# Performance work log

Measured on AMD Instinct MI355X. Metric: run time of the kernel, lower is better.

Reference implementation:

```python
import jax, jax.numpy as jnp
import numpy as np

BETA = 5.0  # init kwarg beta

def _row_normalize(x):
    # torch: diag(1/||x||_2) @ x  == row-wise L2 normalize (O(n*d), no n x n diag)
    return x / jnp.linalg.norm(x, axis=1, keepdims=True)

def _cluster(x, mu, num_iter, beta):
    # The torch code normalizes twice (before and after the init branch);
    # second normalize is idempotent but kept for faithfulness (cheap).
    x = _row_normalize(_row_normalize(x))
    for _ in range(num_iter):  # small fixed iteration count, not a data dim
        r = jax.nn.softmax(beta * (x @ mu.T), axis=1)      # [n, k]
        cluster_r = r.sum(axis=0)                          # [k]
        # torch: diag(1/cluster_r) @ (r.T @ x)  -> row scale of [k, d]
        mu = (r.T @ x) / cluster_r[:, None]                # [k, d]
    r = jax.nn.softmax(beta * (x @ mu.T), axis=1)
    return mu, r

def setup_inputs() -> dict:
    key = jax.random.key(0)
    k1, k2 = jax.random.split(key)
    x = jax.random.normal(k1, (100000, 512), dtype=jnp.float32)        # embeddings [n, d]
    init_mu = jax.random.uniform(k2, (128, 512), dtype=jnp.float32)    # self.init = rand(k, out_dim)
    return {"x": x, "init_mu": init_mu, "num_iter": 2}

def reference(x, init_mu, num_iter):
    mu_init, _ = _cluster(x, init_mu, num_iter, BETA)
    # torch: mu_init.detach().clone() -> stop_gradient
    mu, r = _cluster(x, jax.lax.stop_gradient(mu_init), 1, BETA)
    return (mu, r)
```

## Files before the change

kernel.cpp:

```cpp
#include <hip/hip_runtime.h>
#include <math.h>

constexpr int D = 512;
constexpr int KCL = 128;
constexpr float BETA_C = 5.0f;
constexpr int GSPLIT = 256;

typedef __attribute__((ext_vector_type(8))) short short8;
typedef __attribute__((ext_vector_type(4))) float f32x4;

typedef const __attribute__((address_space(1))) unsigned int* gptr_t;
typedef __attribute__((address_space(3))) unsigned int* sptr_t;

static __device__ __forceinline__ unsigned short f2bf(float f) {
    unsigned u = __builtin_bit_cast(unsigned, f);
    unsigned r = (u + 0x7FFFu + ((u >> 16) & 1u)) >> 16;
    return (unsigned short)r;
}
static __device__ __forceinline__ float bf2f(unsigned short h) {
    unsigned u = ((unsigned)h) << 16;
    return __builtin_bit_cast(float, u);
}
static __device__ __forceinline__ void split_bf(float v, unsigned short& h, unsigned short& lo) {
    h = f2bf(v);
    lo = f2bf(v - bf2f(h));
}

__global__ __launch_bounds__(256) void conv_x_kernel(const float* __restrict__ x,
        unsigned short* __restrict__ xh, unsigned short* __restrict__ xl,
        float* __restrict__ inv_norm, int n)
{
    int row  = blockIdx.x * 4 + (threadIdx.x >> 6);
    int lane = threadIdx.x & 63;
    if (row >= n) return;
    const float4* xr = reinterpret_cast<const float4*>(x + (size_t)row * D);
    float4 f0 = xr[lane];
    float4 f1 = xr[lane + 64];
    float s = f0.x*f0.x + f0.y*f0.y + f0.z*f0.z + f0.w*f0.w
            + f1.x*f1.x + f1.y*f1.y + f1.z*f1.z + f1.w*f1.w;
    #pragma unroll
    for (int m = 32; m; m >>= 1) s += __shfl_xor(s, m, 64);
    if (lane == 0) inv_norm[row] = 1.0f / sqrtf(s);

    ushort4 h0, l0, h1, l1;
    split_bf(f0.x, h0.x, l0.x); split_bf(f0.y, h0.y, l0.y);
    split_bf(f0.z, h0.z, l0.z); split_bf(f0.w, h0.w, l0.w);
    split_bf(f1.x, h1.x, l1.x); split_bf(f1.y, h1.y, l1.y);
    split_bf(f1.z, h1.z, l1.z); split_bf(f1.w, h1.w, l1.w);

    ushort4* xhr = reinterpret_cast<ushort4*>(xh + (size_t)row * D);
    ushort4* xlr = reinterpret_cast<ushort4*>(xl + (size_t)row * D);
    xhr[lane]      = h0;
    xhr[lane + 64] = h1;
    xlr[lane]      = l0;
    xlr[lane + 64] = l1;
}

__global__ __launch_bounds__(256) void conv_mu_kernel(const float* __restrict__ mu,
        unsigned short* __restrict__ mh, unsigned short* __restrict__ ml)
{
    int i = blockIdx.x * 256 + threadIdx.x;
    float4 v = reinterpret_cast<const float4*>(mu)[i];
    ushort4 h, l;
    split_bf(v.x, h.x, l.x); split_bf(v.y, h.y, l.y);
    split_bf(v.z, h.z, l.z); split_bf(v.w, h.w, l.w);
    reinterpret_cast<ushort4*>(mh)[i] = h;
    reinterpret_cast<ushort4*>(ml)[i] = l;
}

template<bool FIN>
__global__ __launch_bounds__(256) void passA_mfma_kernel(
    const unsigned short* __restrict__ xh, const unsigned short* __restrict__ xl,
    const unsigned short* __restrict__ mh, const unsigned short* __restrict__ ml,
    const float* __restrict__ inv_norm, float* __restrict__ r_out,
    float* __restrict__ cluster_r, int n)
{
    __shared__ unsigned short lds[4][128 * 32];
    __shared__ float part[4 * 128];

    const int t  = threadIdx.x;
    const int w  = t >> 6;
    const int l  = t & 63;
    const int fr = l & 15;
    const int fb = (l >> 4) * 8;
    const int rowBase = blockIdx.x * 128;

    f32x4 acc[2][8];
    #pragma unroll
    for (int m = 0; m < 2; ++m)
        #pragma unroll
        for (int nn = 0; nn < 8; ++nn) acc[m][nn] = (f32x4){0.f, 0.f, 0.f, 0.f};

    const unsigned short* pAh[2]; const unsigned short* pAl[2];
    const unsigned short* pBh[2]; const unsigned short* pBl[2];
    #pragma unroll
    for (int u = 0; u < 2; ++u) {
        int c = t + u * 256;
        int row = c >> 2;
        int kc  = (c & 3) * 8;
        int ga  = min(rowBase + row, n - 1);
        pAh[u] = xh + (size_t)ga * D + kc;
        pAl[u] = xl + (size_t)ga * D + kc;
        pBh[u] = mh + (size_t)row * D + kc;
        pBl[u] = ml + (size_t)row * D + kc;
    }

    for (int kb = 0; kb < D; kb += 32) {
        #pragma unroll
        for (int u = 0; u < 2; ++u) {
            int c = t + u * 256;
            __builtin_amdgcn_global_load_lds((gptr_t)pAh[u], (sptr_t)&lds[0][c * 8], 16, 0, 0);
            __builtin_amdgcn_global_load_lds((gptr_t)pAl[u], (sptr_t)&lds[1][c * 8], 16, 0, 0);
            __builtin_amdgcn_global_load_lds((gptr_t)pBh[u], (sptr_t)&lds[2][c * 8], 16, 0, 0);
            __builtin_amdgcn_global_load_lds((gptr_t)pBl[u], (sptr_t)&lds[3][c * 8], 16, 0, 0);
            pAh[u] += 32; pAl[u] += 32; pBh[u] += 32; pBl[u] += 32;
        }
        __syncthreads();

        short8 ah0 = *reinterpret_cast<const short8*>(&lds[0][(w * 32 +  0 + fr) * 32 + fb]);
        short8 ah1 = *reinterpret_cast<const short8*>(&lds[0][(w * 32 + 16 + fr) * 32 + fb]);
        short8 al0 = *reinterpret_cast<const short8*>(&lds[1][(w * 32 +  0 + fr) * 32 + fb]);
        short8 al1 = *reinterpret_cast<const short8*>(&lds[1][(w * 32 + 16 + fr) * 32 + fb]);
        #pragma unroll
        for (int nn = 0; nn < 8; ++nn) {
            short8 bh = *reinterpret_cast<const short8*>(&lds[2][(nn * 16 + fr) * 32 + fb]);
            short8 bl = *reinterpret_cast<const short8*>(&lds[3][(nn * 16 + fr) * 32 + fb]);
            acc[0][nn] = __builtin_amdgcn_mfma_f32_16x16x32_bf16(ah0, bh, acc[0][nn], 0, 0, 0);
            acc[1][nn] = __builtin_amdgcn_mfma_f32_16x16x32_bf16(ah1, bh, acc[1][nn], 0, 0, 0);
            acc[0][nn] = __builtin_amdgcn_mfma_f32_16x16x32_bf16(ah0, bl, acc[0][nn], 0, 0, 0);
            acc[1][nn] = __builtin_amdgcn_mfma_f32_16x16x32_bf16(ah1, bl, acc[1][nn], 0, 0, 0);
            acc[0][nn] = __builtin_amdgcn_mfma_f32_16x16x32_bf16(al0, bh, acc[0][nn], 0, 0, 0);
            acc[1][nn] = __builtin_amdgcn_mfma_f32_16x16x32_bf16(al1, bh, acc[1][nn], 0, 0, 0);
        }
        __syncthreads();
    }

    float csum[8];
    #pragma unroll
    for (int nn = 0; nn < 8; ++nn) csum[nn] = 0.f;

    #pragma unroll
    for (int m = 0; m < 2; ++m) {
        #pragma unroll
        for (int rr = 0; rr < 4; ++rr) {
            int row = rowBase + w * 32 + m * 16 + (l >> 4) * 4 + rr;
            bool valid = row < n;
            float sv = inv_norm[min(row, n - 1)];
            float bs = BETA_C * sv;
            float lg[8];
            float mx = -3.0e38f;
            #pragma unroll
            for (int nn = 0; nn < 8; ++nn) { lg[nn] = bs * acc[m][nn][rr]; mx = fmaxf(mx, lg[nn]); }
            #pragma unroll
            for (int sh = 1; sh < 16; sh <<= 1) mx = fmaxf(mx, __shfl_xor(mx, sh, 64));
            float e[8];
            float sum = 0.f;
            #pragma unroll
            for (int nn = 0; nn < 8; ++nn) { e[nn] = __expf(lg[nn] - mx); sum += e[nn]; }
            #pragma unroll
            for (int sh = 1; sh < 16; sh <<= 1) sum += __shfl_xor(sum, sh, 64);
            float rinv = 1.0f / sum;
            if (valid) {
                float* ro = r_out + (size_t)row * KCL + fr;
                if (!FIN) {
                    #pragma unroll
                    for (int nn = 0; nn < 8; ++nn) {
                        float rv = e[nn] * rinv;
                        csum[nn] += rv;
                        ro[nn * 16] = rv * sv;
                    }
                } else {
                    #pragma unroll
                    for (int nn = 0; nn < 8; ++nn) ro[nn * 16] = e[nn] * rinv;
                }
            }
        }
    }

    if (!FIN) {
        #pragma unroll
        for (int nn = 0; nn < 8; ++nn) {
            csum[nn] += __shfl_xor(csum[nn], 16, 64);
            csum[nn] += __shfl_xor(csum[nn], 32, 64);
        }
        if (l < 16) {
            #pragma unroll
            for (int nn = 0; nn < 8; ++nn) part[w * 128 + nn * 16 + l] = csum[nn];
        }
        __syncthreads();
        if (t < 128) {
            atomicAdd(&cluster_r[t], part[t] + part[128 + t] + part[256 + t] + part[384 + t]);
        }
    }
}

__global__ __launch_bounds__(256) void passB_kernel(
    const float* __restrict__ rp, const float* __restrict__ x,
    float* __restrict__ partials, int n, int chunk)
{
    __shared__ float Rs[32 * 132];
    __shared__ float Xs[32 * 132];

    const int t = threadIdx.x;
    const int a = t >> 4;
    const int b = t & 15;
    const int dbase = blockIdx.x * 128;
    const int r0 = blockIdx.y * chunk;
    const int r1 = min(n, r0 + chunk);

    float acc[8][8];
    #pragma unroll
    for (int i = 0; i < 8; ++i)
        #pragma unroll
        for (int j = 0; j < 8; ++j) acc[i][j] = 0.f;

    for (int ib = r0; ib < r1; ib += 32) {
        #pragma unroll
        for (int u = 0; u < 4; ++u) {
            int f  = t + u * 256;
            int ii = f >> 5;
            int c4 = (f & 31) << 2;
            int gr = ib + ii;
            float4 rv = make_float4(0.f, 0.f, 0.f, 0.f);
            float4 xv = make_float4(0.f, 0.f, 0.f, 0.f);
            if (gr < r1) {
                rv = *reinterpret_cast<const float4*>(rp + (size_t)gr * KCL + c4);
                xv = *reinterpret_cast<const float4*>(x + (size_t)gr * D + dbase + c4);
            }
            *reinterpret_cast<float4*>(&Rs[ii * 132 + c4]) = rv;
            *reinterpret_cast<float4*>(&Xs[ii * 132 + c4]) = xv;
        }
        __syncthreads();
        #pragma unroll 4
        for (int ii = 0; ii < 32; ++ii) {
            float4 rv0 = *reinterpret_cast<const float4*>(&Rs[ii * 132 + a * 8]);
            float4 rv1 = *reinterpret_cast<const float4*>(&Rs[ii * 132 + a * 8 + 4]);
            float4 xv0 = *reinterpret_cast<const float4*>(&Xs[ii * 132 + b * 4]);
            float4 xv1 = *reinterpret_cast<const float4*>(&Xs[ii * 132 + 64 + b * 4]);
            float rr[8] = {rv0.x, rv0.y, rv0.z, rv0.w, rv1.x, rv1.y, rv1.z, rv1.w};
            #pragma unroll
            for (int i = 0; i < 8; ++i) {
                acc[i][0] += rr[i] * xv0.x;
                acc[i][1] += rr[i] * xv0.y;
                acc[i][2] += rr[i] * xv0.z;
                acc[i][3] += rr[i] * xv0.w;
                acc[i][4] += rr[i] * xv1.x;
                acc[i][5] += rr[i] * xv1.y;
                acc[i][6] += rr[i] * xv1.z;
                acc[i][7] += rr[i] * xv1.w;
            }
        }
        __syncthreads();
    }

    float* pb = partials + (size_t)blockIdx.y * (KCL * D);
    #pragma unroll
    for (int i = 0; i < 8; ++i) {
        int c = a * 8 + i;
        float4 o0 = make_float4(acc[i][0], acc[i][1], acc[i][2], acc[i][3]);
        float4 o1 = make_float4(acc[i][4], acc[i][5], acc[i][6], acc[i][7]);
        *reinterpret_cast<float4*>(pb + (size_t)c * D + dbase + b * 4)      = o0;
        *reinterpret_cast<float4*>(pb + (size_t)c * D + dbase + 64 + b * 4) = o1;
    }
}

__global__ __launch_bounds__(256) void reduce_kernel(
    const float* __restrict__ partials, const float* __restrict__ cluster_r,
    float* __restrict__ mu_out, unsigned short* __restrict__ mh, unsigned short* __restrict__ ml)
{
    int idx = blockIdx.x * 256 + threadIdx.x;
    float s = 0.f;
    #pragma unroll 8
    for (int g = 0; g < GSPLIT; ++g) s += partials[(size_t)g * (KCL * D) + idx];
    int c = idx >> 9;
    float m = s / cluster_r[c];
    mu_out[idx] = m;
    unsigned short h, lo;
    split_bf(m, h, lo);
    mh[idx] = h;
    ml[idx] = lo;
}

extern "C" void kernel_launch(void* const* d_in, const int* in_sizes, int n_in,
                              void* d_out, int out_size, void* d_ws, size_t ws_size,
                              hipStream_t stream)
{
    const float* x   = (const float*)d_in[0];
    const float* mu0 = (const float*)d_in[1];
    const int n = in_sizes[0] / D;

    char* ws = (char*)d_ws;
    size_t off = 0;
    auto alloc = [&](size_t bytes) { size_t cur = off; off += (bytes + 255) & ~(size_t)255; return cur; };
    float*          inv_norm = (float*)(ws + alloc((size_t)n * 4));
    float*          r_ws     = (float*)(ws + alloc((size_t)n * KCL * 4));
    float*          parts    = (float*)(ws + alloc((size_t)GSPLIT * KCL * D * 4));
    float*          cr       = (float*)(ws + alloc(512));
    float*          mu_a     = (float*)(ws + alloc((size_t)KCL * D * 4));
    float*          mu_b     = (float*)(ws + alloc((size_t)KCL * D * 4));
    unsigned short* xh       = (unsigned short*)(ws + alloc((size_t)n * D * 2));
    unsigned short* xl       = (unsigned short*)(ws + alloc((size_t)n * D * 2));
    unsigned short* muh      = (unsigned short*)(ws + alloc((size_t)KCL * D * 2));
    unsigned short* mul      = (unsigned short*)(ws + alloc((size_t)KCL * D * 2));

    float* mu_final = (float*)d_out;
    float* r_final  = (float*)d_out + KCL * D;

    const int chunk   = (n + GSPLIT - 1) / GSPLIT;
    const int ablocks = (n + 127) / 128;

    conv_x_kernel<<<dim3((n + 3) / 4), 256, 0, stream>>>(x, xh, xl, inv_norm, n);
    conv_mu_kernel<<<dim3((KCL * D) / 1024), 256, 0, stream>>>(mu0, muh, mul);

    float* mu_tgt[3] = {mu_a, mu_b, mu_final};
    for (int it = 0; it < 3; ++it) {
        hipMemsetAsync(cr, 0, 512, stream);
        passA_mfma_kernel<false><<<dim3(ablocks), 256, 0, stream>>>(xh, xl, muh, mul, inv_norm, r_ws, cr, n);
        passB_kernel<<<dim3(4, GSPLIT), 256, 0, stream>>>(r_ws, x, parts, n, chunk);
        reduce_kernel<<<dim3((KCL * D) / 256), 256, 0, stream>>>(parts, cr, mu_tgt[it], muh, mul);
    }
    passA_mfma_kernel<true><<<dim3(ablocks), 256, 0, stream>>>(xh, xl, muh, mul, inv_norm, r_final, nullptr, n);
}
```

Measured before the change: 1.231 ms.

## Move r^T·x accumulation to split-bf16 MFMA with transposed packed operands

The FP32 FMA passB is replaced by an MFMA kernel that reads transposed, hi/lo-packed bf16 copies of r and x, computing r^T·x with three bf16 MFMAs per product. PassA now loads fp32 x directly and splits it on the fly, and its epilogue writes r transposed and packed through LDS. The precomputed xh/xl row-major buffers are dropped and the split count is halved. This is meant to remove the scalar FP32 GEMM cost of passB, at the price of an extra transpose-conversion pass, padding, and slightly reduced precision from the split-bf16 scheme.

```diff
diff --git a/kernel.cpp b/kernel.cpp
--- a/kernel.cpp
+++ b/kernel.cpp
@@ -4,7 +4,7 @@
 constexpr int D = 512;
 constexpr int KCL = 128;
 constexpr float BETA_C = 5.0f;
-constexpr int GSPLIT = 256;
+constexpr int SPLIT = 128;
 
 typedef __attribute__((ext_vector_type(8))) short short8;
 typedef __attribute__((ext_vector_type(4))) float f32x4;
@@ -21,39 +21,94 @@
     unsigned u = ((unsigned)h) << 16;
     return __builtin_bit_cast(float, u);
 }
-static __device__ __forceinline__ void split_bf(float v, unsigned short& h, unsigned short& lo) {
-    h = f2bf(v);
-    lo = f2bf(v - bf2f(h));
-}
-
-__global__ __launch_bounds__(256) void conv_x_kernel(const float* __restrict__ x,
-        unsigned short* __restrict__ xh, unsigned short* __restrict__ xl,
+static __device__ __forceinline__ unsigned pack_split(float v) {
+    unsigned short h = f2bf(v);
+    float hf = bf2f(h);
+    unsigned short lo = f2bf(v - hf);
+    return (unsigned)h | ((unsigned)lo << 16);
+}
+
+static __device__ __forceinline__ void split8(float4 a, float4 b, short8& hi, short8& lo) {
+    float v[8] = {a.x, a.y, a.z, a.w, b.x, b.y, b.z, b.w};
+    union { unsigned short us[8]; short8 s8; } H, L;
+    #pragma unroll
+    for (int j = 0; j < 8; ++j) {
+        unsigned short h = f2bf(v[j]);
+        float hf = bf2f(h);
+        H.us[j] = h;
+        L.us[j] = f2bf(v[j] - hf);
+    }
+    hi = H.s8; lo = L.s8;
+}
+
+static __device__ __forceinline__ void unpack8(uint4 a, uint4 b, short8& hi, short8& lo) {
+    union { unsigned u[4]; short8 s8; } H, L;
+    H.u[0] = (a.x & 0xFFFFu) | (a.y << 16);
+    H.u[1] = (a.z & 0xFFFFu) | (a.w << 16);
+    H.u[2] = (b.x & 0xFFFFu) | (b.y << 16);
+    H.u[3] = (b.z & 0xFFFFu) | (b.w << 16);
+    L.u[0] = (a.x >> 16) | (a.y & 0xFFFF0000u);
+    L.u[1] = (a.z >> 16) | (a.w & 0xFFFF0000u);
+    L.u[2] = (b.x >> 16) | (b.y & 0xFFFF0000u);
+    L.u[3] = (b.z >> 16) | (b.w & 0xFFFF0000u);
+    hi = H.s8; lo = L.s8;
+}
+
+__global__ __launch_bounds__(256) void conv_xT_kernel(const float* __restrict__ x,
+        unsigned* __restrict__ xt, float* __restrict__ normp, int n, int npad)
+{
+    __shared__ float tile[64 * 132];
+    const int t = threadIdx.x;
+    const int kbase = blockIdx.x * 64;
+    const int dbase = blockIdx.y * 128;
+
+    #pragma unroll
+    for (int u = 0; u < 8; ++u) {
+        int f = t + u * 256;
+        int row = f >> 5;
+        int c4 = (f & 31) << 2;
+        int gk = kbase + row;
+        float4 v = make_float4(0.f, 0.f, 0.f, 0.f);
+        if (gk < n) v = *reinterpret_cast<const float4*>(x + (size_t)gk * D + dbase + c4);
+        *reinterpret_cast<float4*>(&tile[row * 132 + c4]) = v;
+    }
+    __syncthreads();
+
+    if (t < 64) {
+        int gk = kbase + t;
+        if (gk < n) {
+            float s = 0.f;
+            #pragma unroll
+            for (int j = 0; j < 128; ++j) {
+                float v = tile[t * 132 + ((j + t) & 127)];
+                s += v * v;
+            }
+            normp[(size_t)blockIdx.y * n + gk] = s;
+        }
+    }
+
+    int dl = t >> 1, kh = t & 1;
+    size_t gb = (size_t)(dbase + dl) * npad + kbase + kh * 32;
+    #pragma unroll
+    for (int q = 0; q < 8; ++q) {
+        uint4 o;
+        unsigned* op = reinterpret_cast<unsigned*>(&o);
+        #pragma unroll
+        for (int j = 0; j < 4; ++j) {
+            float v = tile[(kh * 32 + q * 4 + j) * 132 + dl];
+            op[j] = pack_split(v);
+        }
+        *reinterpret_cast<uint4*>(xt + gb + q * 4) = o;
+    }
+}
+
+__global__ __launch_bounds__(256) void norm_fin_kernel(const float* __restrict__ normp,
         float* __restrict__ inv_norm, int n)
 {
-    int row  = blockIdx.x * 4 + (threadIdx.x >> 6);
-    int lane = threadIdx.x & 63;
-    if (row >= n) return;
-    const float4* xr = reinterpret_cast<const float4*>(x + (size_t)row * D);
-    float4 f0 = xr[lane];
-    float4 f1 = xr[lane + 64];
-    float s = f0.x*f0.x + f0.y*f0.y + f0.z*f0.z + f0.w*f0.w
-            + f1.x*f1.x + f1.y*f1.y + f1.z*f1.z + f1.w*f1.w;
-    #pragma unroll
-    for (int m = 32; m; m >>= 1) s += __shfl_xor(s, m, 64);
-    if (lane == 0) inv_norm[row] = 1.0f / sqrtf(s);
-
-    ushort4 h0, l0, h1, l1;
-    split_bf(f0.x, h0.x, l0.x); split_bf(f0.y, h0.y, l0.y);
-    split_bf(f0.z, h0.z, l0.z); split_bf(f0.w, h0.w, l0.w);
-    split_bf(f1.x, h1.x, l1.x); split_bf(f1.y, h1.y, l1.y);
-    split_bf(f1.z, h1.z, l1.z); split_bf(f1.w, h1.w, l1.w);
-
-    ushort4* xhr = reinterpret_cast<ushort4*>(xh + (size_t)row * D);
-    ushort4* xlr = reinterpret_cast<ushort4*>(xl + (size_t)row * D);
-    xhr[lane]      = h0;
-    xhr[lane + 64] = h1;
-    xlr[lane]      = l0;
-    xlr[lane + 64] = l1;
+    int i = blockIdx.x * 256 + threadIdx.x;
+    if (i < n)
+        inv_norm[i] = 1.0f / sqrtf(normp[i] + normp[(size_t)n + i] +
+                                   normp[2 * (size_t)n + i] + normp[3 * (size_t)n + i]);
 }
 
 __global__ __launch_bounds__(256) void conv_mu_kernel(const float* __restrict__ mu,
@@ -62,27 +117,44 @@
     int i = blockIdx.x * 256 + threadIdx.x;
     float4 v = reinterpret_cast<const float4*>(mu)[i];
     ushort4 h, l;
-    split_bf(v.x, h.x, l.x); split_bf(v.y, h.y, l.y);
-    split_bf(v.z, h.z, l.z); split_bf(v.w, h.w, l.w);
+    float hf;
+    h.x = f2bf(v.x); hf = bf2f(h.x); l.x = f2bf(v.x - hf);
+    h.y = f2bf(v.y); hf = bf2f(h.y); l.y = f2bf(v.y - hf);
+    h.z = f2bf(v.z); hf = bf2f(h.z); l.z = f2bf(v.z - hf);
+    h.w = f2bf(v.w); hf = bf2f(h.w); l.w = f2bf(v.w - hf);
     reinterpret_cast<ushort4*>(mh)[i] = h;
     reinterpret_cast<ushort4*>(ml)[i] = l;
 }
 
+__global__ __launch_bounds__(256) void pad_r_kernel(unsigned* __restrict__ rt, int npad, int k0)
+{
+    int cnt = npad - k0;
+    int idx = blockIdx.x * 256 + threadIdx.x;
+    if (idx < KCL * cnt) {
+        int cl = idx / cnt;
+        int k  = idx - cl * cnt;
+        rt[(size_t)cl * npad + k0 + k] = 0u;
+    }
+}
+
 template<bool FIN>
 __global__ __launch_bounds__(256) void passA_mfma_kernel(
-    const unsigned short* __restrict__ xh, const unsigned short* __restrict__ xl,
+    const float* __restrict__ x,
     const unsigned short* __restrict__ mh, const unsigned short* __restrict__ ml,
     const float* __restrict__ inv_norm, float* __restrict__ r_out,
-    float* __restrict__ cluster_r, int n)
-{
-    __shared__ unsigned short lds[4][128 * 32];
+    unsigned* __restrict__ r_tp, float* __restrict__ cluster_r, int n, int npad)
+{
+    __shared__ union {
+        struct { float a[128 * 32]; unsigned short bh[128 * 32]; unsigned short bl[128 * 32]; } c;
+        unsigned T[64 * 130];
+    } lds;
     __shared__ float part[4 * 128];
 
     const int t  = threadIdx.x;
     const int w  = t >> 6;
     const int l  = t & 63;
     const int fr = l & 15;
-    const int fb = (l >> 4) * 8;
+    const int g  = l >> 4;
     const int rowBase = blockIdx.x * 128;
 
     f32x4 acc[2][8];
@@ -91,40 +163,58 @@
         #pragma unroll
         for (int nn = 0; nn < 8; ++nn) acc[m][nn] = (f32x4){0.f, 0.f, 0.f, 0.f};
 
-    const unsigned short* pAh[2]; const unsigned short* pAl[2];
-    const unsigned short* pBh[2]; const unsigned short* pBl[2];
+    const float* pA[4];
+    const unsigned short* pBh[2];
+    const unsigned short* pBl[2];
+    #pragma unroll
+    for (int u = 0; u < 4; ++u) {
+        int c   = t + u * 256;
+        int row = c >> 3;
+        int ch  = c & 7;
+        int ga  = min(rowBase + row, n - 1);
+        pA[u] = x + (size_t)ga * D + ((ch ^ (row & 7)) << 2);
+    }
     #pragma unroll
     for (int u = 0; u < 2; ++u) {
-        int c = t + u * 256;
+        int c   = t + u * 256;
         int row = c >> 2;
-        int kc  = (c & 3) * 8;
-        int ga  = min(rowBase + row, n - 1);
-        pAh[u] = xh + (size_t)ga * D + kc;
-        pAl[u] = xl + (size_t)ga * D + kc;
-        pBh[u] = mh + (size_t)row * D + kc;
-        pBl[u] = ml + (size_t)row * D + kc;
+        int ch  = c & 3;
+        pBh[u] = mh + row * D + ch * 8;
+        pBl[u] = ml + row * D + ch * 8;
     }
 
     for (int kb = 0; kb < D; kb += 32) {
+        #pragma unroll
+        for (int u = 0; u < 4; ++u) {
+            int c = t + u * 256;
+            __builtin_amdgcn_global_load_lds((gptr_t)pA[u], (sptr_t)&lds.c.a[c * 4], 16, 0, 0);
+            pA[u] += 32;
+        }
         #pragma unroll
         for (int u = 0; u < 2; ++u) {
             int c = t + u * 256;
-            __builtin_amdgcn_global_load_lds((gptr_t)pAh[u], (sptr_t)&lds[0][c * 8], 16, 0, 0);
-            __builtin_amdgcn_global_load_lds((gptr_t)pAl[u], (sptr_t)&lds[1][c * 8], 16, 0, 0);
-            __builtin_amdgcn_global_load_lds((gptr_t)pBh[u], (sptr_t)&lds[2][c * 8], 16, 0, 0);
-            __builtin_amdgcn_global_load_lds((gptr_t)pBl[u], (sptr_t)&lds[3][c * 8], 16, 0, 0);
-            pAh[u] += 32; pAl[u] += 32; pBh[u] += 32; pBl[u] += 32;
+            __builtin_amdgcn_global_load_lds((gptr_t)pBh[u], (sptr_t)&lds.c.bh[c * 8], 16, 0, 0);
+            __builtin_amdgcn_global_load_lds((gptr_t)pBl[u], (sptr_t)&lds.c.bl[c * 8], 16, 0, 0);
+            pBh[u] += 32; pBl[u] += 32;
         }
         __syncthreads();
 
-        short8 ah0 = *reinterpret_cast<const short8*>(&lds[0][(w * 32 +  0 + fr) * 32 + fb]);
-        short8 ah1 = *reinterpret_cast<const short8*>(&lds[0][(w * 32 + 16 + fr) * 32 + fb]);
-        short8 al0 = *reinterpret_cast<const short8*>(&lds[1][(w * 32 +  0 + fr) * 32 + fb]);
-        short8 al1 = *reinterpret_cast<const short8*>(&lds[1][(w * 32 + 16 + fr) * 32 + fb]);
+        const int rA0 = w * 32 + fr;
+        const int rA1 = rA0 + 16;
+        const int msk = fr & 7;
+        float4 q0 = *reinterpret_cast<const float4*>(&lds.c.a[rA0 * 32 + (((2 * g)     ^ msk) << 2)]);
+        float4 q1 = *reinterpret_cast<const float4*>(&lds.c.a[rA0 * 32 + (((2 * g + 1) ^ msk) << 2)]);
+        float4 q2 = *reinterpret_cast<const float4*>(&lds.c.a[rA1 * 32 + (((2 * g)     ^ msk) << 2)]);
+        float4 q3 = *reinterpret_cast<const float4*>(&lds.c.a[rA1 * 32 + (((2 * g + 1) ^ msk) << 2)]);
+        short8 ah0, al0, ah1, al1;
+        split8(q0, q1, ah0, al0);
+        split8(q2, q3, ah1, al1);
+
+        const int fb = g * 8;
         #pragma unroll
         for (int nn = 0; nn < 8; ++nn) {
-            short8 bh = *reinterpret_cast<const short8*>(&lds[2][(nn * 16 + fr) * 32 + fb]);
-            short8 bl = *reinterpret_cast<const short8*>(&lds[3][(nn * 16 + fr) * 32 + fb]);
+            short8 bh = *reinterpret_cast<const short8*>(&lds.c.bh[(nn * 16 + fr) * 32 + fb]);
+            short8 bl = *reinterpret_cast<const short8*>(&lds.c.bl[(nn * 16 + fr) * 32 + fb]);
             acc[0][nn] = __builtin_amdgcn_mfma_f32_16x16x32_bf16(ah0, bh, acc[0][nn], 0, 0, 0);
             acc[1][nn] = __builtin_amdgcn_mfma_f32_16x16x32_bf16(ah1, bh, acc[1][nn], 0, 0, 0);
             acc[0][nn] = __builtin_amdgcn_mfma_f32_16x16x32_bf16(ah0, bl, acc[0][nn], 0, 0, 0);
@@ -143,7 +233,7 @@
     for (int m = 0; m < 2; ++m) {
         #pragma unroll
         for (int rr = 0; rr < 4; ++rr) {
-            int row = rowBase + w * 32 + m * 16 + (l >> 4) * 4 + rr;
+            int row = rowBase + w * 32 + m * 16 + g * 4 + rr;
             bool valid = row < n;
             float sv = inv_norm[min(row, n - 1)];
             float bs = BETA_C * sv;
@@ -160,20 +250,45 @@
             #pragma unroll
             for (int sh = 1; sh < 16; sh <<= 1) sum += __shfl_xor(sum, sh, 64);
             float rinv = 1.0f / sum;
-            if (valid) {
-                float* ro = r_out + (size_t)row * KCL + fr;
-                if (!FIN) {
-                    #pragma unroll
-                    for (int nn = 0; nn < 8; ++nn) {
-                        float rv = e[nn] * rinv;
-                        csum[nn] += rv;
-                        ro[nn * 16] = rv * sv;
-                    }
-                } else {
+
+            if (FIN) {
+                if (valid) {
+                    float* ro = r_out + (size_t)row * KCL + fr;
                     #pragma unroll
                     for (int nn = 0; nn < 8; ++nn) ro[nn * 16] = e[nn] * rinv;
                 }
+            } else {
+                int trow = w * 16 + g * 4 + rr;
+                #pragma unroll
+                for (int nn = 0; nn < 8; ++nn) {
+                    unsigned wv = 0u;
+                    if (valid) {
+                        float rv = e[nn] * rinv;
+                        csum[nn] += rv;
+                        wv = pack_split(rv * sv);
+                    }
+                    lds.T[trow * 130 + nn * 16 + fr] = wv;
+                }
             }
+        }
+        if (!FIN) {
+            __syncthreads();
+            #pragma unroll
+            for (int u = 0; u < 2; ++u) {
+                int item = t + u * 256;
+                int cl = item >> 2;
+                int q  = item & 3;
+                #pragma unroll
+                for (int wg = 0; wg < 4; ++wg) {
+                    uint4 v;
+                    v.x = lds.T[(wg * 16 + q * 4 + 0) * 130 + cl];
+                    v.y = lds.T[(wg * 16 + q * 4 + 1) * 130 + cl];
+                    v.z = lds.T[(wg * 16 + q * 4 + 2) * 130 + cl];
+                    v.w = lds.T[(wg * 16 + q * 4 + 3) * 130 + cl];
+                    *reinterpret_cast<uint4*>(r_tp + (size_t)cl * npad + rowBase + wg * 32 + m * 16 + q * 4) = v;
+                }
+            }
+            __syncthreads();
         }
     }
 
@@ -194,91 +309,103 @@
     }
 }
 
-__global__ __launch_bounds__(256) void passB_kernel(
-    const float* __restrict__ rp, const float* __restrict__ x,
-    float* __restrict__ partials, int n, int chunk)
-{
-    __shared__ float Rs[32 * 132];
-    __shared__ float Xs[32 * 132];
-
-    const int t = threadIdx.x;
-    const int a = t >> 4;
-    const int b = t & 15;
+__global__ __launch_bounds__(256) void passB_mfma_kernel(
+    const unsigned* __restrict__ rt, const unsigned* __restrict__ xt,
+    float* __restrict__ partials, int npad, int chunk)
+{
+    __shared__ __align__(16) unsigned ldsR[128 * 32];
+    __shared__ __align__(16) unsigned ldsX[128 * 32];
+
+    const int t  = threadIdx.x;
+    const int w  = t >> 6;
+    const int l  = t & 63;
+    const int fr = l & 15;
+    const int g  = l >> 4;
     const int dbase = blockIdx.x * 128;
-    const int r0 = blockIdx.y * chunk;
-    const int r1 = min(n, r0 + chunk);
-
-    float acc[8][8];
-    #pragma unroll
-    for (int i = 0; i < 8; ++i)
-        #pragma unroll
-        for (int j = 0; j < 8; ++j) acc[i][j] = 0.f;
-
-    for (int ib = r0; ib < r1; ib += 32) {
+    const int s  = blockIdx.y;
+    const int k0 = s * chunk;
+
+    f32x4 acc[2][8];
+    #pragma unroll
+    for (int m = 0; m < 2; ++m)
+        #pragma unroll
+        for (int nn = 0; nn < 8; ++nn) acc[m][nn] = (f32x4){0.f, 0.f, 0.f, 0.f};
+
+    const unsigned* pR[4];
+    const unsigned* pX[4];
+    #pragma unroll
+    for (int u = 0; u < 4; ++u) {
+        int c   = t + u * 256;
+        int row = c >> 3;
+        int ch  = c & 7;
+        int koff = (ch ^ (row & 7)) << 2;
+        pR[u] = rt + (size_t)row * npad + k0 + koff;
+        pX[u] = xt + (size_t)(dbase + row) * npad + k0 + koff;
+    }
+
+    for (int kb = 0; kb < chunk; kb += 32) {
         #pragma unroll
         for (int u = 0; u < 4; ++u) {
-            int f  = t + u * 256;
-            int ii = f >> 5;
-            int c4 = (f & 31) << 2;
-            int gr = ib + ii;
-            float4 rv = make_float4(0.f, 0.f, 0.f, 0.f);
-            float4 xv = make_float4(0.f, 0.f, 0.f, 0.f);
-            if (gr < r1) {
-                rv = *reinterpret_cast<const float4*>(rp + (size_t)gr * KCL + c4);
-                xv = *reinterpret_cast<const float4*>(x + (size_t)gr * D + dbase + c4);
+            int c = t + u * 256;
+            __builtin_amdgcn_global_load_lds((gptr_t)pR[u], (sptr_t)&ldsR[c * 4], 16, 0, 0);
+            __builtin_amdgcn_global_load_lds((gptr_t)pX[u], (sptr_t)&ldsX[c * 4], 16, 0, 0);
+            pR[u] += 32; pX[u] += 32;
+        }
+        __syncthreads();
+
+        const int msk = fr & 7;
+        short8 rh[2], rl[2];
+        #pragma unroll
+        for (int m = 0; m < 2; ++m) {
+            int r0 = w * 32 + m * 16 + fr;
+            uint4 a0 = *reinterpret_cast<const uint4*>(&ldsR[r0 * 32 + (((2 * g)     ^ msk) << 2)]);
+            uint4 a1 = *reinterpret_cast<const uint4*>(&ldsR[r0 * 32 + (((2 * g + 1) ^ msk) << 2)]);
+            unpack8(a0, a1, rh[m], rl[m]);
+        }
+        #pragma unroll
+        for (int nn = 0; nn < 8; ++nn) {
+            int rb = nn * 16 + fr;
+            uint4 b0 = *reinterpret_cast<const uint4*>(&ldsX[rb * 32 + (((2 * g)     ^ msk) << 2)]);
+            uint4 b1 = *reinterpret_cast<const uint4*>(&ldsX[rb * 32 + (((2 * g + 1) ^ msk) << 2)]);
+            short8 xh, xl;
+            unpack8(b0, b1, xh, xl);
+            #pragma unroll
+            for (int m = 0; m < 2; ++m) {
+                acc[m][nn] = __builtin_amdgcn_mfma_f32_16x16x32_bf16(rh[m], xh, acc[m][nn], 0, 0, 0);
+                acc[m][nn] = __builtin_amdgcn_mfma_f32_16x16x32_bf16(rh[m], xl, acc[m][nn], 0, 0, 0);
+                acc[m][nn] = __builtin_amdgcn_mfma_f32_16x16x32_bf16(rl[m], xh, acc[m][nn], 0, 0, 0);
             }
-            *reinterpret_cast<float4*>(&Rs[ii * 132 + c4]) = rv;
-            *reinterpret_cast<float4*>(&Xs[ii * 132 + c4]) = xv;
         }
         __syncthreads();
-        #pragma unroll 4
-        for (int ii = 0; ii < 32; ++ii) {
-            float4 rv0 = *reinterpret_cast<const float4*>(&Rs[ii * 132 + a * 8]);
-            float4 rv1 = *reinterpret_cast<const float4*>(&Rs[ii * 132 + a * 8 + 4]);
-            float4 xv0 = *reinterpret_cast<const float4*>(&Xs[ii * 132 + b * 4]);
-            float4 xv1 = *reinterpret_cast<const float4*>(&Xs[ii * 132 + 64 + b * 4]);
-            float rr[8] = {rv0.x, rv0.y, rv0.z, rv0.w, rv1.x, rv1.y, rv1.z, rv1.w};
-            #pragma unroll
-            for (int i = 0; i < 8; ++i) {
-                acc[i][0] += rr[i] * xv0.x;
-                acc[i][1] += rr[i] * xv0.y;
-                acc[i][2] += rr[i] * xv0.z;
-                acc[i][3] += rr[i] * xv0.w;
-                acc[i][4] += rr[i] * xv1.x;
-                acc[i][5] += rr[i] * xv1.y;
-                acc[i][6] += rr[i] * xv1.z;
-                acc[i][7] += rr[i] * xv1.w;
+    }
+
+    float* pb = partials + (size_t)s * (KCL * D);
+    #pragma unroll
+    for (int m = 0; m < 2; ++m)
+        #pragma unroll
+        for (int nn = 0; nn < 8; ++nn)
+            #pragma unroll
+            for (int q = 0; q < 4; ++q) {
+                int cl = w * 32 + m * 16 + g * 4 + q;
+                pb[(size_t)cl * D + dbase + nn * 16 + fr] = acc[m][nn][q];
             }
-        }
-        __syncthreads();
-    }
-
-    float* pb = partials + (size_t)blockIdx.y * (KCL * D);
-    #pragma unroll
-    for (int i = 0; i < 8; ++i) {
-        int c = a * 8 + i;
-        float4 o0 = make_float4(acc[i][0], acc[i][1], acc[i][2], acc[i][3]);
-        float4 o1 = make_float4(acc[i][4], acc[i][5], acc[i][6], acc[i][7]);
-        *reinterpret_cast<float4*>(pb + (size_t)c * D + dbase + b * 4)      = o0;
-        *reinterpret_cast<float4*>(pb + (size_t)c * D + dbase + 64 + b * 4) = o1;
-    }
 }
 
 __global__ __launch_bounds__(256) void reduce_kernel(
     const float* __restrict__ partials, const float* __restrict__ cluster_r,
-    float* __restrict__ mu_out, unsigned short* __restrict__ mh, unsigned short* __restrict__ ml)
+    float* __restrict__ mu_out, unsigned short* __restrict__ mh, unsigned short* __restrict__ ml,
+    int gsplit)
 {
     int idx = blockIdx.x * 256 + threadIdx.x;
     float s = 0.f;
-    #pragma unroll 8
-    for (int g = 0; g < GSPLIT; ++g) s += partials[(size_t)g * (KCL * D) + idx];
+    for (int g = 0; g < gsplit; ++g) s += partials[(size_t)g * (KCL * D) + idx];
     int c = idx >> 9;
     float m = s / cluster_r[c];
     mu_out[idx] = m;
-    unsigned short h, lo;
-    split_bf(m, h, lo);
+    unsigned short h = f2bf(m);
+    float hf = bf2f(h);
     mh[idx] = h;
-    ml[idx] = lo;
+    ml[idx] = f2bf(m - hf);
 }
 
 extern "C" void kernel_launch(void* const* d_in, const int* in_sizes, int n_in,
@@ -288,36 +415,47 @@
     const float* x   = (const float*)d_in[0];
     const float* mu0 = (const float*)d_in[1];
     const int n = in_sizes[0] / D;
+
+    const int chunk   = ((n + SPLIT * 32 - 1) / (SPLIT * 32)) * 32;
+    const int npad    = SPLIT * chunk;
+    const int ablocks = (n + 127) / 128;
+    const int KT      = npad / 64;
 
     char* ws = (char*)d_ws;
     size_t off = 0;
     auto alloc = [&](size_t bytes) { size_t cur = off; off += (bytes + 255) & ~(size_t)255; return cur; };
     float*          inv_norm = (float*)(ws + alloc((size_t)n * 4));
-    float*          r_ws     = (float*)(ws + alloc((size_t)n * KCL * 4));
-    float*          parts    = (float*)(ws + alloc((size_t)GSPLIT * KCL * D * 4));
+    float*          normp    = (float*)(ws + alloc((size_t)4 * n * 4));
+    unsigned*       r_tp     = (unsigned*)(ws + alloc((size_t)KCL * npad * 4));
+    unsigned*       xT_p     = (unsigned*)(ws + alloc((size_t)D * npad * 4));
+    float*          parts    = (float*)(ws + alloc((size_t)SPLIT * KCL * D * 4));
     float*          cr       = (float*)(ws + alloc(512));
     float*          mu_a     = (float*)(ws + alloc((size_t)KCL * D * 4));
-    float*          mu_b     = (float*)(ws + alloc((size_t)KCL * D * 4));
-    unsigned short* xh       = (unsigned short*)(ws + alloc((size_t)n * D * 2));
-    unsigned short* xl       = (unsigned short*)(ws + alloc((size_t)n * D * 2));
     unsigned short* muh      = (unsigned short*)(ws + alloc((size_t)KCL * D * 2));
     unsigned short* mul      = (unsigned short*)(ws + alloc((size_t)KCL * D * 2));
 
     float* mu_final = (float*)d_out;
     float* r_final  = (float*)d_out + KCL * D;
 
-    const int chunk   = (n + GSPLIT - 1) / GSPLIT;
-    const int ablocks = (n + 127) / 128;
-
-    conv_x_kernel<<<dim3((n + 3) / 4), 256, 0, stream>>>(x, xh, xl, inv_norm, n);
+    conv_xT_kernel<<<dim3(KT, 4), 256, 0, stream>>>(x, xT_p, normp, n, npad);
+    norm_fin_kernel<<<dim3((n + 255) / 256), 256, 0, stream>>>(normp, inv_norm, n);
     conv_mu_kernel<<<dim3((KCL * D) / 1024), 256, 0, stream>>>(mu0, muh, mul);
-
-    float* mu_tgt[3] = {mu_a, mu_b, mu_final};
+    {
+        int k0 = ablocks * 128;
+        int cnt = npad - k0;
+        int tot = KCL * cnt;
+        if (tot > 0)
+            pad_r_kernel<<<dim3((tot + 255) / 256), 256, 0, stream>>>(r_tp, npad, k0);
+    }
+
+    float* mu_tgt[3] = {mu_a, mu_a, mu_final};
     for (int it = 0; it < 3; ++it) {
         hipMemsetAsync(cr, 0, 512, stream);
-        passA_mfma_kernel<false><<<dim3(ablocks), 256, 0, stream>>>(xh, xl, muh, mul, inv_norm, r_ws, cr, n);
-        passB_kernel<<<dim3(4, GSPLIT), 256, 0, stream>>>(r_ws, x, parts, n, chunk);
-        reduce_kernel<<<dim3((KCL * D) / 256), 256, 0, stream>>>(parts, cr, mu_tgt[it], muh, mul);
-    }
-    passA_mfma_kernel<true><<<dim3(ablocks), 256, 0, stream>>>(xh, xl, muh, mul, inv_norm, r_final, nullptr, n);
-}
+        passA_mfma_kernel<false><<<dim3(ablocks), 256, 0, stream>>>(
+            x, muh, mul, inv_norm, nullptr, r_tp, cr, n, npad);
+        passB_mfma_kernel<<<dim3(4, SPLIT), 256, 0, stream>>>(r_tp, xT_p, parts, npad, chunk);
+        reduce_kernel<<<dim3((KCL * D) / 256), 256, 0, stream>>>(parts, cr, mu_tgt[it], muh, mul, SPLIT);
+    }
+    passA_mfma_kernel<true><<<dim3(ablocks), 256, 0, stream>>>(
+        x, muh, mul, inv_norm, r_final, nullptr, nullptr, n, npad);
+}
```

Result: slower. 1.389 ms (+12.8%).
